# Kernel optimization log

Measured on AMD Instinct MI355X. Metric: run time of the kernel, lower is better.

The kernel has to match this reference:

```python
import jax, jax.numpy as jnp
import numpy as np

B, D, N, H = 4, 256, 2048, 4
HEAD_DIM = D // H


def conv1x1(W, b, x):
    # Conv1d(kernel_size=1): [B, Cin, N] -> [B, Cout, N]
    return jnp.einsum('oi,bin->bon', W, x) + b[None, :, None]


def setup_inputs() -> dict:
    key = jax.random.key(0)
    ks = jax.random.split(key, 8)
    s = 0.05
    return {
        'x': jax.random.normal(ks[0], (B, D, N), jnp.float32),
        'source': jax.random.normal(ks[1], (B, D, N), jnp.float32),
        'edge': jax.random.uniform(ks[2], (B, N, N), jnp.float32),
        'Wq': jax.random.normal(ks[3], (D, D), jnp.float32) * s,
        'bq': jnp.zeros((D,), jnp.float32),
        'Wk': jax.random.normal(ks[4], (D, D), jnp.float32) * s,
        'bk': jnp.zeros((D,), jnp.float32),
        'Wv': jax.random.normal(ks[5], (D, D), jnp.float32) * s,
        'bv': jnp.zeros((D,), jnp.float32),
        'Wm': jax.random.normal(ks[6], (D, D), jnp.float32) * s,
        'bm': jnp.zeros((D,), jnp.float32),
        'W1': jax.random.normal(ks[7], (2 * D, 2 * D), jnp.float32) * s,
        'b1': jnp.zeros((2 * D,), jnp.float32),
        'W2': jax.random.normal(jax.random.fold_in(key, 99), (D, 2 * D), jnp.float32) * s,
        'b2': jnp.zeros((D,), jnp.float32),
    }


def reference(x, source, edge, Wq, bq, Wk, bk, Wv, bv, Wm, bm, W1, b1, W2, b2):
    b = x.shape[0]
    # projections, then split channels D -> (head_dim, H), matching torch .view
    q = conv1x1(Wq, bq, x).reshape(b, HEAD_DIM, H, -1)       # [B, d, H, N]
    k = conv1x1(Wk, bk, source).reshape(b, HEAD_DIM, H, -1)  # [B, d, H, M]
    v = conv1x1(Wv, bv, source).reshape(b, HEAD_DIM, H, -1)
    scores = jnp.einsum('bdhn,bdhm->bhnm', q, k) / jnp.sqrt(jnp.float32(HEAD_DIM))
    prob = jax.nn.softmax(scores, axis=-1) * edge[:, None, :, :]  # edge-weighted probs
    msg = jnp.einsum('bhnm,bdhm->bdhn', prob, v).reshape(b, D, -1)
    message = conv1x1(Wm, bm, msg)                           # merge heads
    h = jnp.concatenate([x, message], axis=1)                # [B, 2D, N]
    h = jax.nn.relu(conv1x1(W1, b1, h))
    return conv1x1(W2, b2, h)                                # [B, D, N]
```

## Files before the change

kernel.cpp:

```cpp
#include <hip/hip_runtime.h>
#include <math.h>

#define B_ 4
#define D_ 256
#define N_ 2048
#define H_ 4

typedef __attribute__((ext_vector_type(8))) __bf16 bf16x8;
typedef __attribute__((ext_vector_type(4))) __bf16 bf16x4;
typedef __attribute__((ext_vector_type(4))) float f32x4;

__device__ __forceinline__ void load_row16(const float* src, bf16x8* xs) {
    float tmp[16];
    *(float4*)&tmp[0]  = *(const float4*)&src[0];
    *(float4*)&tmp[4]  = *(const float4*)&src[4];
    *(float4*)&tmp[8]  = *(const float4*)&src[8];
    *(float4*)&tmp[12] = *(const float4*)&src[12];
    __bf16* o = (__bf16*)xs;
#pragma unroll
    for (int i = 0; i < 16; ++i) o[i] = (__bf16)tmp[i];
}
__device__ __forceinline__ void load_row16(const __bf16* src, bf16x8* xs) {
    xs[0] = *(const bf16x8*)src;
    xs[1] = *(const bf16x8*)(src + 8);
}

template <typename In1T, typename In2T, typename OutT>
__device__ __forceinline__ void conv_tile(
    const In1T* __restrict__ in1, int C1,
    const In2T* __restrict__ in2, int C2,
    const float* __restrict__ Wt, const float* __restrict__ bias,
    OutT* __restrict__ out, int Cout, int K, int RELU, float oscale,
    int b, int o0, int n0, __bf16 (*sXT)[72])
{
    const int t = threadIdx.x;
    const int w  = t >> 6;
    const int g  = (t >> 4) & 3;
    const int c16 = t & 15;
    const int d_ld = t & 63;
    const int xcol = (t >> 6) * 16;

    f32x4 acc[4];
#pragma unroll
    for (int i = 0; i < 4; ++i) acc[i] = (f32x4){0.f, 0.f, 0.f, 0.f};

    bf16x8 xs[2];
    float4 wreg[4];
    const int ow = o0 + 16 * w + c16;

    auto LOADX = [&](int ks) {
        const int ch = ks + d_ld;
        if (ch < C1) load_row16(in1 + ((size_t)b * C1 + ch) * N_ + n0 + xcol, xs);
        else         load_row16(in2 + ((size_t)b * C2 + (ch - C1)) * N_ + n0 + xcol, xs);
    };
    auto LOADW = [&](int ks) {
        wreg[0] = *(const float4*)&Wt[(size_t)ow * K + ks + 8 * g];
        wreg[1] = *(const float4*)&Wt[(size_t)ow * K + ks + 8 * g + 4];
        wreg[2] = *(const float4*)&Wt[(size_t)ow * K + ks + 32 + 8 * g];
        wreg[3] = *(const float4*)&Wt[(size_t)ow * K + ks + 32 + 8 * g + 4];
    };
    auto WRITEXT = [&](int buf) {
        __bf16 (*sx)[72] = sXT + (size_t)buf * 64;
        const __bf16* kp = (const __bf16*)xs;
#pragma unroll
        for (int i = 0; i < 16; ++i)
            sx[xcol + i][d_ld] = kp[i];
    };

    LOADX(0);
    LOADW(0);
    WRITEXT(0);
    __syncthreads();

    const int nsteps = K >> 6;
    for (int s = 0; s < nsteps; ++s) {
        const int cur = s & 1;
        const int ks = s << 6;
        if (s + 1 < nsteps) LOADX(ks + 64);

        bf16x8 af[2];
#pragma unroll
        for (int kc = 0; kc < 2; ++kc) {
            const float* w0 = (const float*)&wreg[2 * kc];
            const float* w1 = (const float*)&wreg[2 * kc + 1];
#pragma unroll
            for (int i = 0; i < 4; ++i) {
                af[kc][i]     = (__bf16)w0[i];
                af[kc][i + 4] = (__bf16)w1[i];
            }
        }
        if (s + 1 < nsteps) LOADW(ks + 64);

        __bf16 (*sx)[72] = sXT + (size_t)cur * 64;
#pragma unroll
        for (int kc = 0; kc < 2; ++kc)
#pragma unroll
            for (int nsub = 0; nsub < 4; ++nsub) {
                const bf16x8 bfr = *(const bf16x8*)&sx[16 * nsub + c16][32 * kc + 8 * g];
                acc[nsub] = __builtin_amdgcn_mfma_f32_16x16x32_bf16(af[kc], bfr, acc[nsub], 0, 0, 0);
            }

        if (s + 1 < nsteps) WRITEXT(cur ^ 1);
        __syncthreads();
    }

#pragma unroll
    for (int nsub = 0; nsub < 4; ++nsub)
#pragma unroll
        for (int r = 0; r < 4; ++r) {
            const int o = o0 + 16 * w + 4 * g + r;
            float v = acc[nsub][r] + bias[o];
            if (RELU) v = fmaxf(v, 0.f);
            v *= oscale;
            out[((size_t)b * Cout + o) * N_ + n0 + 16 * nsub + c16] = (OutT)v;
        }
}

template <int NS>
__global__ __launch_bounds__(256) void conv_msg_kernel(
    const __bf16* __restrict__ OP, const float* __restrict__ ML,
    const float* __restrict__ Wt, const float* __restrict__ bias,
    __bf16* __restrict__ out)
{
    __shared__ __bf16 sXT[2 * 64][72];
    const int t = threadIdx.x;
    const int w  = t >> 6;
    const int g  = (t >> 4) & 3;
    const int c16 = t & 15;
    const int d_ld = t & 63;
    const int xcol = (t >> 6) * 16;
    const int nt = blockIdx.x;
    const int n0 = nt * 64;
    const int o0 = blockIdx.y * 64;
    const int b  = blockIdx.z;
    const int K = D_, Cout = D_;

    const int h = d_ld & 3;
    const size_t pid0 = ((size_t)(b * H_ + h) * NS) * 32 + nt;

    float invL[16];
#pragma unroll
    for (int i = 0; i < 16; i += 4) {
        float4 a = *(const float4*)&ML[pid0 * 128 + 64 + xcol + i];
        if (NS == 2) {
            const float4 c = *(const float4*)&ML[(pid0 + 32) * 128 + 64 + xcol + i];
            a.x += c.x; a.y += c.y; a.z += c.z; a.w += c.w;
        }
        invL[i + 0] = 1.0f / a.x; invL[i + 1] = 1.0f / a.y;
        invL[i + 2] = 1.0f / a.z; invL[i + 3] = 1.0f / a.w;
    }

    f32x4 acc[4];
#pragma unroll
    for (int i = 0; i < 4; ++i) acc[i] = (f32x4){0.f, 0.f, 0.f, 0.f};

    bf16x8 xs[2];
    float4 wreg[4];
    const int ow = o0 + 16 * w + c16;

    auto LOADX = [&](int ks) {
        const int dd = (ks + d_ld) >> 2;
        const __bf16* p0 = &OP[pid0 * 4096 + dd * 64 + xcol];
        const bf16x8 a0 = *(const bf16x8*)p0;
        const bf16x8 a1 = *(const bf16x8*)(p0 + 8);
        bf16x8 b0, b1;
        if (NS == 2) {
            const __bf16* p1 = &OP[(pid0 + 32) * 4096 + dd * 64 + xcol];
            b0 = *(const bf16x8*)p1;
            b1 = *(const bf16x8*)(p1 + 8);
        }
        __bf16* o = (__bf16*)xs;
#pragma unroll
        for (int i = 0; i < 8; ++i) {
            float v = (float)a0[i];
            if (NS == 2) v += (float)b0[i];
            o[i] = (__bf16)(v * invL[i]);
        }
#pragma unroll
        for (int i = 0; i < 8; ++i) {
            float v = (float)a1[i];
            if (NS == 2) v += (float)b1[i];
            o[8 + i] = (__bf16)(v * invL[8 + i]);
        }
    };
    auto LOADW = [&](int ks) {
        wreg[0] = *(const float4*)&Wt[(size_t)ow * K + ks + 8 * g];
        wreg[1] = *(const float4*)&Wt[(size_t)ow * K + ks + 8 * g + 4];
        wreg[2] = *(const float4*)&Wt[(size_t)ow * K + ks + 32 + 8 * g];
        wreg[3] = *(const float4*)&Wt[(size_t)ow * K + ks + 32 + 8 * g + 4];
    };
    auto WRITEXT = [&](int buf) {
        __bf16 (*sx)[72] = sXT + (size_t)buf * 64;
        const __bf16* kp = (const __bf16*)xs;
#pragma unroll
        for (int i = 0; i < 16; ++i)
            sx[xcol + i][d_ld] = kp[i];
    };

    LOADX(0);
    LOADW(0);
    WRITEXT(0);
    __syncthreads();

    const int nsteps = K >> 6;
    for (int s = 0; s < nsteps; ++s) {
        const int cur = s & 1;
        const int ks = s << 6;
        if (s + 1 < nsteps) LOADX(ks + 64);

        bf16x8 af[2];
#pragma unroll
        for (int kc = 0; kc < 2; ++kc) {
            const float* w0 = (const float*)&wreg[2 * kc];
            const float* w1 = (const float*)&wreg[2 * kc + 1];
#pragma unroll
            for (int i = 0; i < 4; ++i) {
                af[kc][i]     = (__bf16)w0[i];
                af[kc][i + 4] = (__bf16)w1[i];
            }
        }
        if (s + 1 < nsteps) LOADW(ks + 64);

        __bf16 (*sx)[72] = sXT + (size_t)cur * 64;
#pragma unroll
        for (int kc = 0; kc < 2; ++kc)
#pragma unroll
            for (int nsub = 0; nsub < 4; ++nsub) {
                const bf16x8 bfr = *(const bf16x8*)&sx[16 * nsub + c16][32 * kc + 8 * g];
                acc[nsub] = __builtin_amdgcn_mfma_f32_16x16x32_bf16(af[kc], bfr, acc[nsub], 0, 0, 0);
            }

        if (s + 1 < nsteps) WRITEXT(cur ^ 1);
        __syncthreads();
    }

#pragma unroll
    for (int nsub = 0; nsub < 4; ++nsub)
#pragma unroll
        for (int r = 0; r < 4; ++r) {
            const int o = o0 + 16 * w + 4 * g + r;
            const float v = acc[nsub][r] + bias[o];
            out[((size_t)b * Cout + o) * N_ + n0 + 16 * nsub + c16] = (__bf16)v;
        }
}

__global__ __launch_bounds__(256) void conv_mix_kernel(
    const __bf16* __restrict__ in1, int C1,
    const __bf16* __restrict__ in2, int C2,
    const float* __restrict__ W, const float* __restrict__ bias,
    __bf16* __restrict__ out, int Cout, int K)
{
    __shared__ __bf16 sXT[2 * 64][72];
    conv_tile<__bf16, __bf16, __bf16>(in1, C1, in2, C2,
        W, bias, out, Cout, K, 1, 1.0f,
        blockIdx.z, blockIdx.y * 64, blockIdx.x * 64, sXT);
}

__global__ __launch_bounds__(256) void conv_hf_kernel(
    const __bf16* __restrict__ in1, const float* __restrict__ W,
    const float* __restrict__ bias, float* __restrict__ out, int Cout, int K)
{
    __shared__ __bf16 sXT[2 * 64][72];
    conv_tile<__bf16, __bf16, float>(in1, K, (const __bf16*)nullptr, 0,
        W, bias, out, Cout, K, 0, 1.0f,
        blockIdx.z, blockIdx.y * 64, blockIdx.x * 64, sXT);
}

__global__ __launch_bounds__(256) void qkv_conv_kernel(
    const float* __restrict__ x, const float* __restrict__ source,
    const float* __restrict__ Wq, const float* __restrict__ bq,
    const float* __restrict__ Wk, const float* __restrict__ bk,
    const float* __restrict__ Wv, const float* __restrict__ bv,
    __bf16* __restrict__ Qo, __bf16* __restrict__ Ko, __bf16* __restrict__ Vo,
    __bf16* __restrict__ Xh)
{
    if (blockIdx.y == 12) {
        const int slot = blockIdx.x * 4 + blockIdx.z;
        const size_t base = (size_t)slot * 16384;
#pragma unroll
        for (int j = 0; j < 16; ++j) {
            const size_t idx = base + j * 1024 + threadIdx.x * 4;
            const float4 v = *(const float4*)&x[idx];
            bf16x4 o;
            o[0] = (__bf16)v.x; o[1] = (__bf16)v.y;
            o[2] = (__bf16)v.z; o[3] = (__bf16)v.w;
            *(bf16x4*)&Xh[idx] = o;
        }
        return;
    }
    __shared__ __bf16 sXT[2 * 64][72];
    const int sel = blockIdx.y >> 2;
    const int o0  = (blockIdx.y & 3) * 64;
    const float* in = (sel == 0) ? x : source;
    const float* W  = (sel == 0) ? Wq : (sel == 1) ? Wk : Wv;
    const float* bs = (sel == 0) ? bq : (sel == 1) ? bk : bv;
    __bf16* out     = (sel == 0) ? Qo : (sel == 1) ? Ko : Vo;
    const float sc  = (sel == 1) ? 0.125f * 1.4426950408889634f : 1.0f;
    conv_tile<float, float, __bf16>(in, D_, (const float*)nullptr, 0,
        W, bs, out, D_, D_, 0, sc,
        blockIdx.z, o0, blockIdx.x * 64, sXT);
}

template <int NSPLIT>
__global__ __launch_bounds__(256, 4) void attn_kernel(
    const __bf16* __restrict__ Qg, const __bf16* __restrict__ Kg,
    const __bf16* __restrict__ Vg, const float* __restrict__ Eg,
    __bf16* __restrict__ OP, float* __restrict__ ML)
{
    const int nt    = blockIdx.x;
    const int n0    = nt * 64;
    const int split = blockIdx.y % NSPLIT;
    const int h     = blockIdx.y / NSPLIT;
    const int b     = blockIdx.z;
    const int t  = threadIdx.x;
    const int w  = t >> 6;
    const int g  = (t >> 4) & 3;
    const int c16 = t & 15;

    const int MT   = 32 / NSPLIT;
    const int m_lo = split * (N_ / NSPLIT);
    const int pid  = ((b * H_ + h) * NSPLIT + split) * 32 + nt;

    __shared__ __bf16 sKT[2][64][72];
    __shared__ __bf16 sP [2][64][72];

    bf16x8 qf[2];
#pragma unroll
    for (int kc = 0; kc < 2; ++kc)
#pragma unroll
        for (int e = 0; e < 8; ++e) {
            const int d = 32 * kc + 8 * g + e;
            qf[kc][e] = Qg[((size_t)b * D_ + d * H_ + h) * N_ + n0 + 16 * w + c16];
        }

    f32x4 acc[4];
#pragma unroll
    for (int i = 0; i < 4; ++i) acc[i] = (f32x4){0.f, 0.f, 0.f, 0.f};
    float Lr[4];
#pragma unroll
    for (int r = 0; r < 4; ++r) Lr[r] = 0.f;

    const int kd = t >> 2;
    const int km = (t & 3) * 16;
    const size_t kbase = ((size_t)b * D_ + kd * H_ + h) * N_ + m_lo + km;
    const size_t vrow  = ((size_t)b * D_ + (16 * w + c16) * H_ + h) * N_ + m_lo;
    const size_t ebase = ((size_t)b * N_ + n0 + 16 * w + 4 * g) * N_ + m_lo + c16;

    bf16x8 kreg[2];
    bf16x8 vreg[2];
    float  ereg[4][4];

    auto LOADK = [&](int m0) {
        kreg[0] = *(const bf16x8*)&Kg[kbase + m0];
        kreg[1] = *(const bf16x8*)&Kg[kbase + m0 + 8];
    };
    auto LOADV = [&](int m0) {
        vreg[0] = *(const bf16x8*)&Vg[vrow + m0 + 8 * g];
        vreg[1] = *(const bf16x8*)&Vg[vrow + m0 + 32 + 8 * g];
    };
    auto LOADE = [&](int m0) {
#pragma unroll
        for (int r = 0; r < 4; ++r)
#pragma unroll
            for (int ms = 0; ms < 4; ++ms)
                ereg[r][ms] = Eg[ebase + (size_t)r * N_ + m0 + 16 * ms];
    };
    const int kcb = kd >> 3, kcw = kd & 7;
    auto WRITEKT = [&](int buf) {
        const __bf16* kp = (const __bf16*)kreg;
#pragma unroll
        for (int i = 0; i < 16; ++i) {
            const int m = km + i;
            sKT[buf][m][(((kcb ^ ((m >> 3) & 7)) << 3) | kcw)] = kp[i];
        }
    };

    LOADK(0);
    LOADV(0);
    LOADE(0);
    WRITEKT(0);
    __syncthreads();

    for (int mt = 0; mt < MT; ++mt) {
        const int cur = mt & 1;
        const int m0n = (mt < MT - 1 ? mt + 1 : mt) * 64;

        const bf16x8 af0 = vreg[0], af1 = vreg[1];
        LOADK(m0n);
        LOADV(m0n);

        f32x4 sfrag[4];
#pragma unroll
        for (int msub = 0; msub < 4; ++msub) {
            const int m   = 16 * msub + c16;
            const int swz = (m >> 3) & 7;
            f32x4 s = (f32x4){0.f, 0.f, 0.f, 0.f};
#pragma unroll
            for (int kc = 0; kc < 2; ++kc) {
                const bf16x8 bfr = *(const bf16x8*)&sKT[cur][m][((4 * kc + g) ^ swz) << 3];
                s = __builtin_amdgcn_mfma_f32_16x16x32_bf16(qf[kc], bfr, s, 0, 0, 0);
            }
            sfrag[msub] = s;
        }

        {
            const int pc_hi = c16 >> 3, pc_lo = c16 & 7;
#pragma unroll
            for (int msub = 0; msub < 4; ++msub) {
#pragma unroll
                for (int r = 0; r < 4; ++r) {
                    const int nloc = 16 * w + 4 * g + r;
                    const int swz  = (nloc >> 3) & 7;
                    const float p = exp2f(sfrag[msub][r]);
                    Lr[r] += p;
                    sP[cur][nloc][((((2 * msub + pc_hi) ^ swz) << 3) | pc_lo)] =
                        (__bf16)(p * ereg[r][msub]);
                }
            }
        }
        LOADE(m0n);

        WRITEKT(cur ^ 1);
        __syncthreads();

#pragma unroll
        for (int nsub = 0; nsub < 4; ++nsub) {
            const int row = 16 * nsub + c16;
            const int swz = (row >> 3) & 7;
            const bf16x8 b0 = *(const bf16x8*)&sP[cur][row][(g ^ swz) << 3];
            acc[nsub] = __builtin_amdgcn_mfma_f32_16x16x32_bf16(af0, b0, acc[nsub], 0, 0, 0);
            const bf16x8 b1 = *(const bf16x8*)&sP[cur][row][((4 + g) ^ swz) << 3];
            acc[nsub] = __builtin_amdgcn_mfma_f32_16x16x32_bf16(af1, b1, acc[nsub], 0, 0, 0);
        }
    }

#pragma unroll
    for (int mask = 1; mask < 16; mask <<= 1)
#pragma unroll
        for (int r = 0; r < 4; ++r) Lr[r] += __shfl_xor(Lr[r], mask);
    if (c16 == 0) {
#pragma unroll
        for (int r = 0; r < 4; ++r) {
            const int nloc = 16 * w + 4 * g + r;
            ML[(size_t)pid * 128 + nloc]      = 0.0f;
            ML[(size_t)pid * 128 + 64 + nloc] = Lr[r];
        }
    }
#pragma unroll
    for (int nsub = 0; nsub < 4; ++nsub)
#pragma unroll
        for (int r = 0; r < 4; ++r) {
            const int dd = 16 * w + 4 * g + r;
            OP[(size_t)pid * 4096 + dd * 64 + 16 * nsub + c16] = (__bf16)acc[nsub][r];
        }
}

extern "C" void kernel_launch(void* const* d_in, const int* in_sizes, int n_in,
                              void* d_out, int out_size, void* d_ws, size_t ws_size,
                              hipStream_t stream) {
    const float* x      = (const float*)d_in[0];
    const float* source = (const float*)d_in[1];
    const float* edge   = (const float*)d_in[2];
    const float* Wq = (const float*)d_in[3];
    const float* bq = (const float*)d_in[4];
    const float* Wk = (const float*)d_in[5];
    const float* bk = (const float*)d_in[6];
    const float* Wv = (const float*)d_in[7];
    const float* bv = (const float*)d_in[8];
    const float* Wm = (const float*)d_in[9];
    const float* bm = (const float*)d_in[10];
    const float* W1 = (const float*)d_in[11];
    const float* b1 = (const float*)d_in[12];
    const float* W2 = (const float*)d_in[13];
    const float* b2 = (const float*)d_in[14];
    float* out = (float*)d_out;

    const size_t BDN = (size_t)B_ * D_ * N_;
    char* p = (char*)d_ws;
    __bf16* Qh  = (__bf16*)(p);
    __bf16* Kh  = (__bf16*)(p + 2 * BDN);
    __bf16* Vh  = (__bf16*)(p + 4 * BDN);
    __bf16* MES = (__bf16*)(p + 6 * BDN);
    __bf16* H1  = (__bf16*)(p + 8 * BDN);
    __bf16* Xh  = (__bf16*)(p + 12 * BDN);
    char*   tail = p + 14 * BDN;
    const size_t baseBytes = 14 * BDN;

    const dim3 blk(256);
    const dim3 gD(N_ / 64, D_ / 64, B_);
    const dim3 g2D(N_ / 64, 2 * D_ / 64, B_);

    auto needFor = [&](int ns) {
        const size_t pids = (size_t)ns * B_ * H_ * 32;
        return baseBytes + pids * 4096 * 2 + pids * 128 * 4;
    };

    const int NS = (ws_size >= needFor(2)) ? 2 : 1;
    const size_t pids = (size_t)NS * B_ * H_ * 32;
    __bf16* OP = (__bf16*)tail;
    float*  ML = (float*)(tail + pids * 4096 * 2);

    qkv_conv_kernel<<<dim3(N_ / 64, 13, B_), blk, 0, stream>>>(
        x, source, Wq, bq, Wk, bk, Wv, bv, Qh, Kh, Vh, Xh);

    if (NS == 2) {
        attn_kernel<2><<<dim3(32, H_ * 2, B_), blk, 0, stream>>>(Qh, Kh, Vh, edge, OP, ML);
        conv_msg_kernel<2><<<gD, blk, 0, stream>>>(OP, ML, Wm, bm, MES);
    } else {
        attn_kernel<1><<<dim3(32, H_, B_), blk, 0, stream>>>(Qh, Kh, Vh, edge, OP, ML);
        conv_msg_kernel<1><<<gD, blk, 0, stream>>>(OP, ML, Wm, bm, MES);
    }

    conv_mix_kernel<<<g2D, blk, 0, stream>>>(Xh, D_, MES, D_, W1, b1, H1, 2 * D_, 2 * D_);
    conv_hf_kernel<<<gD, blk, 0, stream>>>(H1, W2, b2, out, D_, 2 * D_);
}
```

Measured before the change: 126.8 us.

## Add 4-way key split for attention and single-buffer its LDS tiles

```diff
diff --git a/kernel.cpp b/kernel.cpp
--- a/kernel.cpp
+++ b/kernel.cpp
@@ -142,8 +142,9 @@
 #pragma unroll
     for (int i = 0; i < 16; i += 4) {
         float4 a = *(const float4*)&ML[pid0 * 128 + 64 + xcol + i];
-        if (NS == 2) {
-            const float4 c = *(const float4*)&ML[(pid0 + 32) * 128 + 64 + xcol + i];
+#pragma unroll
+        for (int s = 1; s < NS; ++s) {
+            const float4 c = *(const float4*)&ML[(pid0 + (size_t)s * 32) * 128 + 64 + xcol + i];
             a.x += c.x; a.y += c.y; a.z += c.z; a.w += c.w;
         }
         invL[i + 0] = 1.0f / a.x; invL[i + 1] = 1.0f / a.y;
@@ -160,27 +161,22 @@
 
     auto LOADX = [&](int ks) {
         const int dd = (ks + d_ld) >> 2;
-        const __bf16* p0 = &OP[pid0 * 4096 + dd * 64 + xcol];
-        const bf16x8 a0 = *(const bf16x8*)p0;
-        const bf16x8 a1 = *(const bf16x8*)(p0 + 8);
-        bf16x8 b0, b1;
-        if (NS == 2) {
-            const __bf16* p1 = &OP[(pid0 + 32) * 4096 + dd * 64 + xcol];
-            b0 = *(const bf16x8*)p1;
-            b1 = *(const bf16x8*)(p1 + 8);
+        float v0[8], v1[8];
+#pragma unroll
+        for (int i = 0; i < 8; ++i) { v0[i] = 0.f; v1[i] = 0.f; }
+#pragma unroll
+        for (int s = 0; s < NS; ++s) {
+            const __bf16* ps = &OP[(pid0 + (size_t)s * 32) * 4096 + dd * 64 + xcol];
+            const bf16x8 a0 = *(const bf16x8*)ps;
+            const bf16x8 a1 = *(const bf16x8*)(ps + 8);
+#pragma unroll
+            for (int i = 0; i < 8; ++i) { v0[i] += (float)a0[i]; v1[i] += (float)a1[i]; }
         }
         __bf16* o = (__bf16*)xs;
 #pragma unroll
         for (int i = 0; i < 8; ++i) {
-            float v = (float)a0[i];
-            if (NS == 2) v += (float)b0[i];
-            o[i] = (__bf16)(v * invL[i]);
-        }
-#pragma unroll
-        for (int i = 0; i < 8; ++i) {
-            float v = (float)a1[i];
-            if (NS == 2) v += (float)b1[i];
-            o[8 + i] = (__bf16)(v * invL[8 + i]);
+            o[i]     = (__bf16)(v0[i] * invL[i]);
+            o[8 + i] = (__bf16)(v1[i] * invL[8 + i]);
         }
     };
     auto LOADW = [&](int ks) {
@@ -302,7 +298,7 @@
 }
 
 template <int NSPLIT>
-__global__ __launch_bounds__(256, 4) void attn_kernel(
+__global__ __launch_bounds__(256) void attn_kernel(
     const __bf16* __restrict__ Qg, const __bf16* __restrict__ Kg,
     const __bf16* __restrict__ Vg, const float* __restrict__ Eg,
     __bf16* __restrict__ OP, float* __restrict__ ML)
@@ -321,8 +317,8 @@
     const int m_lo = split * (N_ / NSPLIT);
     const int pid  = ((b * H_ + h) * NSPLIT + split) * 32 + nt;
 
-    __shared__ __bf16 sKT[2][64][72];
-    __shared__ __bf16 sP [2][64][72];
+    __shared__ __bf16 sKT[64][72];
+    __shared__ __bf16 sP [64][72];
 
     bf16x8 qf[2];
 #pragma unroll
@@ -366,23 +362,22 @@
                 ereg[r][ms] = Eg[ebase + (size_t)r * N_ + m0 + 16 * ms];
     };
     const int kcb = kd >> 3, kcw = kd & 7;
-    auto WRITEKT = [&](int buf) {
+    auto WRITEKT = [&]() {
         const __bf16* kp = (const __bf16*)kreg;
 #pragma unroll
         for (int i = 0; i < 16; ++i) {
             const int m = km + i;
-            sKT[buf][m][(((kcb ^ ((m >> 3) & 7)) << 3) | kcw)] = kp[i];
+            sKT[m][(((kcb ^ ((m >> 3) & 7)) << 3) | kcw)] = kp[i];
         }
     };
 
     LOADK(0);
     LOADV(0);
     LOADE(0);
-    WRITEKT(0);
+    WRITEKT();
     __syncthreads();
 
     for (int mt = 0; mt < MT; ++mt) {
-        const int cur = mt & 1;
         const int m0n = (mt < MT - 1 ? mt + 1 : mt) * 64;
 
         const bf16x8 af0 = vreg[0], af1 = vreg[1];
@@ -397,7 +392,7 @@
             f32x4 s = (f32x4){0.f, 0.f, 0.f, 0.f};
 #pragma unroll
             for (int kc = 0; kc < 2; ++kc) {
-                const bf16x8 bfr = *(const bf16x8*)&sKT[cur][m][((4 * kc + g) ^ swz) << 3];
+                const bf16x8 bfr = *(const bf16x8*)&sKT[m][((4 * kc + g) ^ swz) << 3];
                 s = __builtin_amdgcn_mfma_f32_16x16x32_bf16(qf[kc], bfr, s, 0, 0, 0);
             }
             sfrag[msub] = s;
@@ -413,25 +408,27 @@
                     const int swz  = (nloc >> 3) & 7;
                     const float p = exp2f(sfrag[msub][r]);
                     Lr[r] += p;
-                    sP[cur][nloc][((((2 * msub + pc_hi) ^ swz) << 3) | pc_lo)] =
+                    sP[nloc][((((2 * msub + pc_hi) ^ swz) << 3) | pc_lo)] =
                         (__bf16)(p * ereg[r][msub]);
                 }
             }
         }
         LOADE(m0n);
 
-        WRITEKT(cur ^ 1);
         __syncthreads();
 
 #pragma unroll
         for (int nsub = 0; nsub < 4; ++nsub) {
             const int row = 16 * nsub + c16;
             const int swz = (row >> 3) & 7;
-            const bf16x8 b0 = *(const bf16x8*)&sP[cur][row][(g ^ swz) << 3];
+            const bf16x8 b0 = *(const bf16x8*)&sP[row][(g ^ swz) << 3];
             acc[nsub] = __builtin_amdgcn_mfma_f32_16x16x32_bf16(af0, b0, acc[nsub], 0, 0, 0);
-            const bf16x8 b1 = *(const bf16x8*)&sP[cur][row][((4 + g) ^ swz) << 3];
+            const bf16x8 b1 = *(const bf16x8*)&sP[row][((4 + g) ^ swz) << 3];
             acc[nsub] = __builtin_amdgcn_mfma_f32_16x16x32_bf16(af1, b1, acc[nsub], 0, 0, 0);
         }
+        WRITEKT();
+
+        __syncthreads();
     }
 
 #pragma unroll
@@ -495,7 +492,7 @@
         return baseBytes + pids * 4096 * 2 + pids * 128 * 4;
     };
 
-    const int NS = (ws_size >= needFor(2)) ? 2 : 1;
+    const int NS = (ws_size >= needFor(4)) ? 4 : (ws_size >= needFor(2)) ? 2 : 1;
     const size_t pids = (size_t)NS * B_ * H_ * 32;
     __bf16* OP = (__bf16*)tail;
     float*  ML = (float*)(tail + pids * 4096 * 2);
@@ -503,7 +500,10 @@
     qkv_conv_kernel<<<dim3(N_ / 64, 13, B_), blk, 0, stream>>>(
         x, source, Wq, bq, Wk, bk, Wv, bv, Qh, Kh, Vh, Xh);
 
-    if (NS == 2) {
+    if (NS == 4) {
+        attn_kernel<4><<<dim3(32, H_ * 4, B_), blk, 0, stream>>>(Qh, Kh, Vh, edge, OP, ML);
+        conv_msg_kernel<4><<<gD, blk, 0, stream>>>(OP, ML, Wm, bm, MES);
+    } else if (NS == 2) {
         attn_kernel<2><<<dim3(32, H_ * 2, B_), blk, 0, stream>>>(Qh, Kh, Vh, edge, OP, ML);
         conv_msg_kernel<2><<<gD, blk, 0, stream>>>(OP, ML, Wm, bm, MES);
     } else {
```

New measurement: 133.7 us. 5.5% more time.
